# Performance work log

Hardware: AMD Instinct MI355X
Metric: run time of the kernel (lower is better)

The kernel has to match this reference:

```python
import jax, jax.numpy as jnp
import numpy as np

N, E = 50000, 600000
IN_C, HID, OUT_C = 256, 128, 2
R, B, L = 7, 8, 3
ALPHA = 0.1


def _rgcn(x, src, dst, etype, comp, basis, root, bias):
    # comp: [R,B], basis: [B,d,d] -> per-relation weights W: [R,d,d]
    n, d = x.shape
    W = jnp.einsum('rb,bdf->rdf', comp, basis)
    # combined (dst, relation) segment id for per-relation mean aggregation
    seg = dst * R + etype
    msg = x[src]  # [E,d] gather
    s = jax.ops.segment_sum(msg, seg, num_segments=n * R)  # [N*R,d]
    cnt = jax.ops.segment_sum(jnp.ones((E,), x.dtype), seg, num_segments=n * R)
    agg = (s / jnp.maximum(cnt, 1.0)[:, None]).reshape(n, R, d)  # per-relation mean
    return x @ root + bias + jnp.einsum('nrd,rdf->nf', agg, W)


def setup_inputs() -> dict:
    key = jax.random.key(0)
    ks = jax.random.split(key, 10)
    sc = 0.05
    x = jax.random.normal(ks[0], (N, IN_C), dtype=jnp.float32)
    edge_index = jax.random.randint(ks[1], (2, E), 0, N)
    edge_type = jax.random.randint(ks[2], (E,), 0, R)
    # GPR temp init: alpha*(1-alpha)^k, last entry (1-alpha)^K
    temp = jnp.asarray(ALPHA * (1.0 - ALPHA) ** np.arange(L + 1), dtype=jnp.float32)
    temp = temp.at[-1].set((1.0 - ALPHA) ** L)
    lin1_w = jax.random.normal(ks[3], (IN_C, HID), jnp.float32) * sc
    lin1_b = jnp.zeros((HID,), jnp.float32)
    lin2_w = jax.random.normal(ks[4], (HID, OUT_C), jnp.float32) * sc
    lin2_b = jnp.zeros((OUT_C,), jnp.float32)
    comps = jax.random.normal(ks[5], (L, R, B), jnp.float32) * sc
    bases = jax.random.normal(ks[6], (L, B, HID, HID), jnp.float32) * sc
    roots = jax.random.normal(ks[7], (L, HID, HID), jnp.float32) * sc
    conv_biases = jnp.zeros((L, HID), jnp.float32)
    return dict(x=x, edge_index=edge_index, edge_type=edge_type, temp=temp,
                lin1_w=lin1_w, lin1_b=lin1_b, lin2_w=lin2_w, lin2_b=lin2_b,
                comps=comps, bases=bases, roots=roots, conv_biases=conv_biases)


def reference(x, edge_index, edge_type, temp, lin1_w, lin1_b, lin2_w, lin2_b,
              comps, bases, roots, conv_biases):
    src, dst = edge_index[0], edge_index[1]
    h = x @ lin1_w + lin1_b
    hidden = h * temp[0]
    cur = hidden
    for i in range(L):
        cur = _rgcn(cur, src, dst, edge_type, comps[i], bases[i], roots[i], conv_biases[i])
        if i < L - 1:
            cur = jax.nn.relu(cur)  # dropout p=0.4 is identity in eval mode
        hidden = hidden + temp[i + 1] * cur
    return hidden @ lin2_w + lin2_b
```

## Files before the change

### kernel.cpp

```cpp
#include <hip/hip_runtime.h>
#include <cstdint>


constexpr int N_NODES  = 50000;
constexpr int E_EDGES  = 600000;
constexpr int R_REL    = 7;
constexpr int HID      = 128;
constexpr int IN_C     = 256;
constexpr int L_LAYERS = 3;
constexpr int AGG_COLS = 896;
constexpr int K_CAT    = 1024;
constexpr int NR       = N_NODES * R_REL;
constexpr int SCANR_BLOCKS = (NR + 255) / 256;
constexpr int WCAT_ELEMS = L_LAYERS * 128 * K_CAT;

#define DEVI __device__ __forceinline__

using short8  = __attribute__((ext_vector_type(8))) short;
using floatx4 = __attribute__((ext_vector_type(4))) float;

DEVI unsigned short f2bf(float f) {
  unsigned u = __float_as_uint(f);
  unsigned r = (u + 0x7FFFu + ((u >> 16) & 1u)) >> 16;
  return (unsigned short)r;
}
DEVI float bf2f(unsigned short h) { return __uint_as_float(((unsigned)h) << 16); }

__global__ __launch_bounds__(256) void prep_weights(
    const float* __restrict__ w1,
    const float* __restrict__ comps,
    const float* __restrict__ bases,
    const float* __restrict__ roots,
    unsigned short* __restrict__ w1T,
    unsigned short* __restrict__ wcat2T)
{
  int t = blockIdx.x * 256 + threadIdx.x;
  if (t < WCAT_ELEMS) {
    int l   = t >> 17;
    int rem = t & 131071;
    int f   = rem >> 10;
    int k   = rem & 1023;
    float v;
    if (k < 128) {
      v = roots[((size_t)l * 128 + k) * 128 + f];
    } else {
      int r = (k - 128) >> 7, d = (k - 128) & 127;
      const float* cp = comps + ((size_t)l * R_REL + r) * 8;
      const float* bp = bases + (((size_t)l * 8) * 128 + d) * 128 + f;
      float s = 0.f;
#pragma unroll
      for (int b = 0; b < 8; ++b) s += cp[b] * bp[(size_t)b * 128 * 128];
      v = s;
    }
    wcat2T[t] = f2bf(v);
  } else {
    int u = t - WCAT_ELEMS;
    if (u < HID * IN_C) {
      int m = u >> 8, k = u & 255;
      w1T[m * IN_C + k] = f2bf(w1[k * HID + m]);
    }
  }
}

__global__ __launch_bounds__(256) void hist_kernel(
    const int* __restrict__ ei, const int* __restrict__ et,
    int* __restrict__ cntRel, int* __restrict__ erank)
{
  int e = blockIdx.x * 256 + threadIdx.x;
  if (e >= E_EDGES) return;
  int seg = ei[E_EDGES + e] * R_REL + et[e];
  erank[e] = atomicAdd(&cntRel[seg], 1);
}

__global__ __launch_bounds__(256) void scanA_kernel(
    const int* __restrict__ cnt, int* __restrict__ tmpOff,
    int* __restrict__ blockSums)
{
  __shared__ int s[256];
  int i = blockIdx.x * 256 + threadIdx.x;
  int v = (i < NR) ? cnt[i] : 0;
  s[threadIdx.x] = v;
  __syncthreads();
#pragma unroll
  for (int d = 1; d < 256; d <<= 1) {
    int t = (threadIdx.x >= d) ? s[threadIdx.x - d] : 0;
    __syncthreads();
    s[threadIdx.x] += t;
    __syncthreads();
  }
  if (i < NR) tmpOff[i] = s[threadIdx.x] - v;
  if (threadIdx.x == 255) blockSums[blockIdx.x] = s[255];
}

__global__ __launch_bounds__(256) void scanB_kernel(int* __restrict__ bs)
{
  __shared__ int s[256];
  __shared__ int carry;
  if (threadIdx.x == 0) carry = 0;
  __syncthreads();
  for (int base = 0; base < SCANR_BLOCKS; base += 256) {
    int cOld = carry;
    int i = base + threadIdx.x;
    int v = (i < SCANR_BLOCKS) ? bs[i] : 0;
    s[threadIdx.x] = v;
    __syncthreads();
#pragma unroll
    for (int d = 1; d < 256; d <<= 1) {
      int t = (threadIdx.x >= d) ? s[threadIdx.x - d] : 0;
      __syncthreads();
      s[threadIdx.x] += t;
      __syncthreads();
    }
    if (i < SCANR_BLOCKS) bs[i] = s[threadIdx.x] - v + cOld;
    __syncthreads();
    if (threadIdx.x == 0) carry = cOld + s[255];
    __syncthreads();
  }
}

__global__ __launch_bounds__(256) void scanC_kernel(
    const int* __restrict__ tmpOff, const int* __restrict__ blockSums,
    int* __restrict__ drs)
{
  int i = blockIdx.x * 256 + threadIdx.x;
  if (i < NR) drs[i] = tmpOff[i] + blockSums[blockIdx.x];
  if (i == 0) drs[NR] = E_EDGES;
}

__global__ __launch_bounds__(256) void place_kernel(
    const int* __restrict__ ei, const int* __restrict__ et,
    const int* __restrict__ drs, const int* __restrict__ erank,
    unsigned short* __restrict__ esrc)
{
  int e = blockIdx.x * 256 + threadIdx.x;
  if (e >= E_EDGES) return;
  int seg = ei[E_EDGES + e] * R_REL + et[e];
  int pos = drs[seg] + erank[e];
  esrc[pos] = (unsigned short)ei[e];
}

constexpr int AGG_NPF = 16;
__global__ __launch_bounds__(256) void agg_reg_kernel(
    const unsigned short* __restrict__ curA,
    const unsigned short* __restrict__ esrc,
    const int* __restrict__ drs,
    unsigned short* __restrict__ aggB)
{
  const int tid  = threadIdx.x;
  const int lane = tid & 63;
  const int dst  = blockIdx.x * 4 + (tid >> 6);
  if (dst >= N_NODES) return;
  const int segBase = dst * R_REL;

  int bnd = drs[segBase + (lane & 7)];
  const int a0    = __shfl(bnd, 0);
  const int total = __shfl(bnd, 7) - a0;

  int pk = 0;
  if (lane < total) pk = (int)esrc[a0 + lane];

  const unsigned* colp = (const unsigned*)curA + lane;
  unsigned* outp = (unsigned*)(aggB + (size_t)dst * AGG_COLS) + lane;

  int r = 0;
  int segStart = 0;
  int segEnd = __shfl(bnd, 1) - a0;
  float sx = 0.f, sy = 0.f;
  int pos = 0;

#define AGG_FLUSH()                                                        \
  while (r < R_REL && segEnd == pos) {                                     \
    int c = segEnd - segStart;                                             \
    float sc = (c > 0) ? 1.0f / (float)c : 0.f;                            \
    unsigned pck = (unsigned)f2bf(sx * sc) | ((unsigned)f2bf(sy * sc) << 16); \
    outp[r * 64] = pck;                                                    \
    sx = 0.f; sy = 0.f;                                                    \
    segStart = segEnd;                                                     \
    ++r;                                                                   \
    segEnd = (r < R_REL) ? (__shfl(bnd, r + 1) - a0) : 0x7FFFFFFF;         \
  }

  AGG_FLUSH();

  for (int base = 0; base < total; base += AGG_NPF) {
    const int cnt = min(total - base, AGG_NPF);
    unsigned v[AGG_NPF];
#pragma unroll
    for (int e = 0; e < AGG_NPF; ++e) {
      if (e < cnt) {
        int idx = base + e;
        int src = (idx < 64) ? __shfl(pk, idx) : (int)esrc[a0 + idx];
        v[e] = colp[src * 64];
      }
    }
#pragma unroll
    for (int e = 0; e < AGG_NPF; ++e) {
      if (e >= cnt) break;
      unsigned u = v[e];
      sx += __uint_as_float(u << 16);
      sy += __uint_as_float(u & 0xFFFF0000u);
      ++pos;
      AGG_FLUSH();
    }
  }
#undef AGG_FLUSH
}

__global__ __launch_bounds__(256) void gemm_lin1(
    const float* __restrict__ x,
    const unsigned short* __restrict__ BT,
    const float* __restrict__ bias,
    const float* __restrict__ temp,
    unsigned short* __restrict__ b0out)
{
  __shared__ unsigned short Atile[64][136];
  __shared__ unsigned short Btile[128][136];
  const int tid  = threadIdx.x;
  const int row0 = blockIdx.x * 64;
  const int lane = tid & 63;
  const int wid  = tid >> 6;
  const int wrow = (wid & 1) * 32;
  const int wcol = (wid >> 1) * 64;
  const int l15  = lane & 15;
  const int quad = lane >> 4;

  floatx4 acc[2][4] = {};

  for (int k0 = 0; k0 < IN_C; k0 += 128) {
#pragma unroll
    for (int it = 0; it < 4; ++it) {
      int chunk = it * 256 + tid;
      int r = chunk >> 4, cc = (chunk & 15) << 3;
      int grow = row0 + r;
      uint4 va = make_uint4(0u, 0u, 0u, 0u);
      if (grow < N_NODES) {
        const float* xp = x + (size_t)grow * IN_C + k0 + cc;
        float4 f0 = *(const float4*)xp;
        float4 f1 = *(const float4*)(xp + 4);
        va.x = (unsigned)f2bf(f0.x) | ((unsigned)f2bf(f0.y) << 16);
        va.y = (unsigned)f2bf(f0.z) | ((unsigned)f2bf(f0.w) << 16);
        va.z = (unsigned)f2bf(f1.x) | ((unsigned)f2bf(f1.y) << 16);
        va.w = (unsigned)f2bf(f1.z) | ((unsigned)f2bf(f1.w) << 16);
      }
      *(uint4*)(&Atile[r][cc]) = va;
    }
#pragma unroll
    for (int it = 0; it < 8; ++it) {
      int chunk = it * 256 + tid;
      int n = chunk >> 4, cc = (chunk & 15) << 3;
      *(uint4*)(&Btile[n][cc]) =
          *(const uint4*)(BT + (size_t)n * IN_C + k0 + cc);
    }
    __syncthreads();
#pragma unroll
    for (int ks = 0; ks < 4; ++ks) {
      int kc = ks * 32 + quad * 8;
      short8 af[2], bfr[4];
#pragma unroll
      for (int i = 0; i < 2; ++i)
        af[i] = *(const short8*)(&Atile[wrow + i * 16 + l15][kc]);
#pragma unroll
      for (int j = 0; j < 4; ++j)
        bfr[j] = *(const short8*)(&Btile[wcol + j * 16 + l15][kc]);
#pragma unroll
      for (int i = 0; i < 2; ++i)
#pragma unroll
        for (int j = 0; j < 4; ++j)
          acc[i][j] = __builtin_amdgcn_mfma_f32_16x16x32_bf16(
              af[i], bfr[j], acc[i][j], 0, 0, 0);
    }
    __syncthreads();
  }

  float t0 = temp[0];
#pragma unroll
  for (int i = 0; i < 2; ++i) {
    int lrow0 = wrow + i * 16 + quad * 4;
#pragma unroll
    for (int j = 0; j < 4; ++j) {
      int gcol = wcol + j * 16 + l15;
      float bb = bias[gcol];
#pragma unroll
      for (int r = 0; r < 4; ++r)
        Atile[lrow0 + r][gcol] = f2bf(t0 * (acc[i][j][r] + bb));
    }
  }
  __syncthreads();
#pragma unroll
  for (int it = 0; it < 4; ++it) {
    int chunk = it * 256 + tid;
    int r = chunk >> 4, cc = (chunk & 15) << 3;
    int grow = row0 + r;
    if (grow < N_NODES)
      *(uint4*)(b0out + (size_t)grow * HID + cc) = *(const uint4*)(&Atile[r][cc]);
  }
}

__global__ __launch_bounds__(256) void gemm_layer(
    const unsigned short* __restrict__ curA,
    const unsigned short* __restrict__ aggB,
    const unsigned short* __restrict__ BT,
    const float* __restrict__ bias,
    unsigned short* __restrict__ bout,
    int layer)
{
  __shared__ unsigned short Btile[128][136];
  const int tid  = threadIdx.x;
  const int row0 = blockIdx.x * 128;
  const int lane = tid & 63;
  const int wid  = tid >> 6;
  const int wrow = (wid & 1) * 64;
  const int wcol = (wid >> 1) * 64;
  const int l15  = lane & 15;
  const int quad = lane >> 4;

  floatx4 acc[4][4] = {};

  for (int p = 0; p < 8; ++p) {
#pragma unroll
    for (int it = 0; it < 8; ++it) {
      int chunk = it * 256 + tid;
      int n = chunk >> 4, cc = (chunk & 15) << 3;
      *(uint4*)(&Btile[n][cc]) =
          *(const uint4*)(BT + (size_t)n * K_CAT + p * 128 + cc);
    }
    __syncthreads();
#pragma unroll
    for (int ks = 0; ks < 4; ++ks) {
      int kc = ks * 32 + quad * 8;
      short8 af[4], bfr[4];
#pragma unroll
      for (int i = 0; i < 4; ++i) {
        int grow = row0 + wrow + i * 16 + l15;
        short8 v = {};
        if (grow < N_NODES) {
          const unsigned short* ap = (p == 0)
              ? curA + (size_t)grow * HID + kc
              : aggB + (size_t)grow * AGG_COLS + (p - 1) * 128 + kc;
          v = *(const short8*)ap;
        }
        af[i] = v;
      }
#pragma unroll
      for (int j = 0; j < 4; ++j)
        bfr[j] = *(const short8*)(&Btile[wcol + j * 16 + l15][kc]);
#pragma unroll
      for (int i = 0; i < 4; ++i)
#pragma unroll
        for (int j = 0; j < 4; ++j)
          acc[i][j] = __builtin_amdgcn_mfma_f32_16x16x32_bf16(
              af[i], bfr[j], acc[i][j], 0, 0, 0);
    }
    __syncthreads();
  }

  const bool isLast = (layer == L_LAYERS - 1);
#pragma unroll
  for (int i = 0; i < 4; ++i) {
    int lrow0 = wrow + i * 16 + quad * 4;
#pragma unroll
    for (int j = 0; j < 4; ++j) {
      int gcol = wcol + j * 16 + l15;
      float bb = bias[gcol];
#pragma unroll
      for (int r = 0; r < 4; ++r) {
        float c = acc[i][j][r] + bb;
        if (!isLast) c = fmaxf(c, 0.f);
        Btile[lrow0 + r][gcol] = f2bf(c);
      }
    }
  }
  __syncthreads();
#pragma unroll
  for (int it = 0; it < 8; ++it) {
    int chunk = it * 256 + tid;
    int r = chunk >> 4, cc = (chunk & 15) << 3;
    int grow = row0 + r;
    if (grow < N_NODES)
      *(uint4*)(bout + (size_t)grow * HID + cc) = *(const uint4*)(&Btile[r][cc]);
  }
}

__global__ __launch_bounds__(256) void final_kernel(
    const unsigned short* __restrict__ b0, const unsigned short* __restrict__ b1,
    const unsigned short* __restrict__ b2v, const unsigned short* __restrict__ b3,
    const float* __restrict__ temp,
    const float* __restrict__ w2, const float* __restrict__ b2bias,
    float* __restrict__ out)
{
  int node = blockIdx.x * 4 + (threadIdx.x >> 6);
  int lane = threadIdx.x & 63;
  if (node >= N_NODES) return;
  float t1 = temp[1], t2 = temp[2], t3 = temp[3];
  size_t base = (size_t)node * 64 + lane;
  unsigned u0 = ((const unsigned*)b0)[base];
  unsigned u1 = ((const unsigned*)b1)[base];
  unsigned u2 = ((const unsigned*)b2v)[base];
  unsigned u3 = ((const unsigned*)b3)[base];
  float hx = bf2f((unsigned short)(u0 & 0xFFFF)) +
             t1 * bf2f((unsigned short)(u1 & 0xFFFF)) +
             t2 * bf2f((unsigned short)(u2 & 0xFFFF)) +
             t3 * bf2f((unsigned short)(u3 & 0xFFFF));
  float hy = bf2f((unsigned short)(u0 >> 16)) +
             t1 * bf2f((unsigned short)(u1 >> 16)) +
             t2 * bf2f((unsigned short)(u2 >> 16)) +
             t3 * bf2f((unsigned short)(u3 >> 16));
  int d0 = lane * 2, d1 = lane * 2 + 1;
  float a0 = hx * w2[d0 * 2 + 0] + hy * w2[d1 * 2 + 0];
  float a1 = hx * w2[d0 * 2 + 1] + hy * w2[d1 * 2 + 1];
#pragma unroll
  for (int off = 32; off > 0; off >>= 1) {
    a0 += __shfl_down(a0, off);
    a1 += __shfl_down(a1, off);
  }
  if (lane == 0) {
    out[node * 2 + 0] = a0 + b2bias[0];
    out[node * 2 + 1] = a1 + b2bias[1];
  }
}

extern "C" void kernel_launch(void* const* d_in, const int* in_sizes, int n_in,
                              void* d_out, int out_size, void* d_ws, size_t ws_size,
                              hipStream_t stream) {
  const float* x     = (const float*)d_in[0];
  const int*   ei    = (const int*)d_in[1];
  const int*   et    = (const int*)d_in[2];
  const float* temp  = (const float*)d_in[3];
  const float* w1    = (const float*)d_in[4];
  const float* b1    = (const float*)d_in[5];
  const float* w2    = (const float*)d_in[6];
  const float* b2    = (const float*)d_in[7];
  const float* comps = (const float*)d_in[8];
  const float* bases = (const float*)d_in[9];
  const float* roots = (const float*)d_in[10];
  const float* cbias = (const float*)d_in[11];

  char* ws = (char*)d_ws;
  size_t off = 0;
  auto take = [&](size_t bytes) {
    char* p = ws + off;
    off = (off + bytes + 255) & ~(size_t)255;
    return p;
  };
  unsigned short* wcat2T = (unsigned short*)take((size_t)WCAT_ELEMS * 2);
  unsigned short* w1T    = (unsigned short*)take((size_t)HID * IN_C * 2);
  int*   cntRel  = (int*)take((size_t)NR * 4);
  int*   tmpOffR = (int*)take((size_t)NR * 4);
  int*   blockSumsR = (int*)take((size_t)SCANR_BLOCKS * 4);
  int*   drs     = (int*)take((size_t)(NR + 1) * 4);
  int*   erank   = (int*)take((size_t)E_EDGES * 4);
  unsigned short* esrc = (unsigned short*)take((size_t)E_EDGES * 2);
  unsigned short* bl[L_LAYERS + 1];
  for (int i = 0; i <= L_LAYERS; ++i)
    bl[i] = (unsigned short*)take((size_t)N_NODES * HID * 2);
  unsigned short* aggB = (unsigned short*)take((size_t)N_NODES * AGG_COLS * 2);

  hipMemsetAsync(cntRel, 0, (size_t)NR * 4, stream);

  hipLaunchKernelGGL(prep_weights,
                     dim3((WCAT_ELEMS + HID * IN_C + 255) / 256), dim3(256),
                     0, stream, w1, comps, bases, roots, w1T, wcat2T);
  hipLaunchKernelGGL(hist_kernel, dim3((E_EDGES + 255) / 256), dim3(256), 0,
                     stream, ei, et, cntRel, erank);
  hipLaunchKernelGGL(scanA_kernel, dim3(SCANR_BLOCKS), dim3(256), 0, stream,
                     cntRel, tmpOffR, blockSumsR);
  hipLaunchKernelGGL(scanB_kernel, dim3(1), dim3(256), 0, stream, blockSumsR);
  hipLaunchKernelGGL(scanC_kernel, dim3(SCANR_BLOCKS), dim3(256), 0, stream,
                     tmpOffR, blockSumsR, drs);
  hipLaunchKernelGGL(place_kernel, dim3((E_EDGES + 255) / 256), dim3(256), 0,
                     stream, ei, et, drs, erank, esrc);

  const int rowBlocks64  = (N_NODES + 63) / 64;
  const int rowBlocks128 = (N_NODES + 127) / 128;
  hipLaunchKernelGGL(gemm_lin1, dim3(rowBlocks64), dim3(256), 0, stream,
                     x, w1T, b1, temp, bl[0]);

  for (int l = 0; l < L_LAYERS; ++l) {
    hipLaunchKernelGGL(agg_reg_kernel, dim3((N_NODES + 3) / 4), dim3(256),
                       0, stream, bl[l], esrc, drs, aggB);
    hipLaunchKernelGGL(gemm_layer, dim3(rowBlocks128), dim3(256), 0, stream,
                       bl[l], aggB, wcat2T + (size_t)l * 128 * K_CAT,
                       cbias + (size_t)l * HID, bl[l + 1], l);
  }

  hipLaunchKernelGGL(final_kernel, dim3((N_NODES + 3) / 4), dim3(256), 0, stream,
                     bl[0], bl[1], bl[2], bl[3], temp, w2, b2, (float*)d_out);
}
```

Before: 478.6 us.

## Transform-then-gather: apply relation weights before aggregating edge messages

Swaps the order of the RGCN layer. Instead of aggregating per-relation means into an N x 896 buffer and running a K=1024 GEMM, each layer first computes the root and seven per-relation transforms (eight N x 128 outputs), then gathers with precomputed per-edge offset and 1/count weight. The root term and bias are added during the gather, which also drops the 896-wide aggregate write and reread. The cost is writing and reading an 8 x N x 128 intermediate and 8-byte edge records instead of 2-byte source ids.

```diff
diff --git a/kernel.cpp b/kernel.cpp
--- a/kernel.cpp
+++ b/kernel.cpp
@@ -8,11 +8,9 @@
 constexpr int HID      = 128;
 constexpr int IN_C     = 256;
 constexpr int L_LAYERS = 3;
-constexpr int AGG_COLS = 896;
-constexpr int K_CAT    = 1024;
 constexpr int NR       = N_NODES * R_REL;
 constexpr int SCANR_BLOCKS = (NR + 255) / 256;
-constexpr int WCAT_ELEMS = L_LAYERS * 128 * K_CAT;
+constexpr int WSLAB_ELEMS = L_LAYERS * 8 * 128 * 128;
 
 #define DEVI __device__ __forceinline__
 
@@ -32,29 +30,31 @@
     const float* __restrict__ bases,
     const float* __restrict__ roots,
     unsigned short* __restrict__ w1T,
-    unsigned short* __restrict__ wcat2T)
+    unsigned short* __restrict__ wslabT)
 {
   int t = blockIdx.x * 256 + threadIdx.x;
-  if (t < WCAT_ELEMS) {
-    int l   = t >> 17;
-    int rem = t & 131071;
-    int f   = rem >> 10;
-    int k   = rem & 1023;
+  if (t < WSLAB_ELEMS) {
+    int l    = t >> 17;
+    int rem  = t & 131071;
+    int s    = rem >> 14;
+    int rem2 = rem & 16383;
+    int f    = rem2 >> 7;
+    int k    = rem2 & 127;
     float v;
-    if (k < 128) {
+    if (s == 0) {
       v = roots[((size_t)l * 128 + k) * 128 + f];
     } else {
-      int r = (k - 128) >> 7, d = (k - 128) & 127;
+      int r = s - 1;
       const float* cp = comps + ((size_t)l * R_REL + r) * 8;
-      const float* bp = bases + (((size_t)l * 8) * 128 + d) * 128 + f;
-      float s = 0.f;
-#pragma unroll
-      for (int b = 0; b < 8; ++b) s += cp[b] * bp[(size_t)b * 128 * 128];
-      v = s;
-    }
-    wcat2T[t] = f2bf(v);
+      const float* bp = bases + (((size_t)l * 8) * 128 + k) * 128 + f;
+      float sacc = 0.f;
+#pragma unroll
+      for (int b = 0; b < 8; ++b) sacc += cp[b] * bp[(size_t)b * 128 * 128];
+      v = sacc;
+    }
+    wslabT[t] = f2bf(v);
   } else {
-    int u = t - WCAT_ELEMS;
+    int u = t - WSLAB_ELEMS;
     if (u < HID * IN_C) {
       int m = u >> 8, k = u & 255;
       w1T[m * IN_C + k] = f2bf(w1[k * HID + m]);
@@ -130,80 +130,18 @@
 __global__ __launch_bounds__(256) void place_kernel(
     const int* __restrict__ ei, const int* __restrict__ et,
     const int* __restrict__ drs, const int* __restrict__ erank,
-    unsigned short* __restrict__ esrc)
+    const int* __restrict__ cntRel,
+    uint2* __restrict__ eoffw)
 {
   int e = blockIdx.x * 256 + threadIdx.x;
   if (e >= E_EDGES) return;
-  int seg = ei[E_EDGES + e] * R_REL + et[e];
+  int src = ei[e];
+  int rel = et[e];
+  int seg = ei[E_EDGES + e] * R_REL + rel;
   int pos = drs[seg] + erank[e];
-  esrc[pos] = (unsigned short)ei[e];
-}
-
-constexpr int AGG_NPF = 16;
-__global__ __launch_bounds__(256) void agg_reg_kernel(
-    const unsigned short* __restrict__ curA,
-    const unsigned short* __restrict__ esrc,
-    const int* __restrict__ drs,
-    unsigned short* __restrict__ aggB)
-{
-  const int tid  = threadIdx.x;
-  const int lane = tid & 63;
-  const int dst  = blockIdx.x * 4 + (tid >> 6);
-  if (dst >= N_NODES) return;
-  const int segBase = dst * R_REL;
-
-  int bnd = drs[segBase + (lane & 7)];
-  const int a0    = __shfl(bnd, 0);
-  const int total = __shfl(bnd, 7) - a0;
-
-  int pk = 0;
-  if (lane < total) pk = (int)esrc[a0 + lane];
-
-  const unsigned* colp = (const unsigned*)curA + lane;
-  unsigned* outp = (unsigned*)(aggB + (size_t)dst * AGG_COLS) + lane;
-
-  int r = 0;
-  int segStart = 0;
-  int segEnd = __shfl(bnd, 1) - a0;
-  float sx = 0.f, sy = 0.f;
-  int pos = 0;
-
-#define AGG_FLUSH()                                                        \
-  while (r < R_REL && segEnd == pos) {                                     \
-    int c = segEnd - segStart;                                             \
-    float sc = (c > 0) ? 1.0f / (float)c : 0.f;                            \
-    unsigned pck = (unsigned)f2bf(sx * sc) | ((unsigned)f2bf(sy * sc) << 16); \
-    outp[r * 64] = pck;                                                    \
-    sx = 0.f; sy = 0.f;                                                    \
-    segStart = segEnd;                                                     \
-    ++r;                                                                   \
-    segEnd = (r < R_REL) ? (__shfl(bnd, r + 1) - a0) : 0x7FFFFFFF;         \
-  }
-
-  AGG_FLUSH();
-
-  for (int base = 0; base < total; base += AGG_NPF) {
-    const int cnt = min(total - base, AGG_NPF);
-    unsigned v[AGG_NPF];
-#pragma unroll
-    for (int e = 0; e < AGG_NPF; ++e) {
-      if (e < cnt) {
-        int idx = base + e;
-        int src = (idx < 64) ? __shfl(pk, idx) : (int)esrc[a0 + idx];
-        v[e] = colp[src * 64];
-      }
-    }
-#pragma unroll
-    for (int e = 0; e < AGG_NPF; ++e) {
-      if (e >= cnt) break;
-      unsigned u = v[e];
-      sx += __uint_as_float(u << 16);
-      sy += __uint_as_float(u & 0xFFFF0000u);
-      ++pos;
-      AGG_FLUSH();
-    }
-  }
-#undef AGG_FLUSH
+  unsigned off = ((1u + (unsigned)rel) * (unsigned)N_NODES + (unsigned)src) * 64u;
+  float w = 1.0f / (float)cntRel[seg];
+  eoffw[pos] = make_uint2(off, __float_as_uint(w));
 }
 
 __global__ __launch_bounds__(256) void gemm_lin1(
@@ -296,17 +234,15 @@
   }
 }
 
-__global__ __launch_bounds__(256) void gemm_layer(
+__global__ __launch_bounds__(256) void tg_kernel(
     const unsigned short* __restrict__ curA,
-    const unsigned short* __restrict__ aggB,
-    const unsigned short* __restrict__ BT,
-    const float* __restrict__ bias,
-    unsigned short* __restrict__ bout,
-    int layer)
+    const unsigned short* __restrict__ WT,
+    unsigned short* __restrict__ T)
 {
   __shared__ unsigned short Btile[128][136];
   const int tid  = threadIdx.x;
   const int row0 = blockIdx.x * 128;
+  const int s    = blockIdx.y;
   const int lane = tid & 63;
   const int wid  = tid >> 6;
   const int wrow = (wid & 1) * 64;
@@ -314,71 +250,126 @@
   const int l15  = lane & 15;
   const int quad = lane >> 4;
 
+  const unsigned short* Wp = WT + (size_t)s * 128 * 128;
+
+#pragma unroll
+  for (int it = 0; it < 8; ++it) {
+    int chunk = it * 256 + tid;
+    int n = chunk >> 4, cc = (chunk & 15) << 3;
+    *(uint4*)(&Btile[n][cc]) = *(const uint4*)(Wp + (size_t)n * 128 + cc);
+  }
+  __syncthreads();
+
   floatx4 acc[4][4] = {};
-
-  for (int p = 0; p < 8; ++p) {
-#pragma unroll
-    for (int it = 0; it < 8; ++it) {
-      int chunk = it * 256 + tid;
-      int n = chunk >> 4, cc = (chunk & 15) << 3;
-      *(uint4*)(&Btile[n][cc]) =
-          *(const uint4*)(BT + (size_t)n * K_CAT + p * 128 + cc);
-    }
-    __syncthreads();
-#pragma unroll
-    for (int ks = 0; ks < 4; ++ks) {
-      int kc = ks * 32 + quad * 8;
-      short8 af[4], bfr[4];
-#pragma unroll
-      for (int i = 0; i < 4; ++i) {
-        int grow = row0 + wrow + i * 16 + l15;
-        short8 v = {};
-        if (grow < N_NODES) {
-          const unsigned short* ap = (p == 0)
-              ? curA + (size_t)grow * HID + kc
-              : aggB + (size_t)grow * AGG_COLS + (p - 1) * 128 + kc;
-          v = *(const short8*)ap;
-        }
-        af[i] = v;
-      }
+#pragma unroll
+  for (int ks = 0; ks < 4; ++ks) {
+    int kc = ks * 32 + quad * 8;
+    short8 af[4], bfr[4];
+#pragma unroll
+    for (int i = 0; i < 4; ++i) {
+      int grow = row0 + wrow + i * 16 + l15;
+      short8 v = {};
+      if (grow < N_NODES)
+        v = *(const short8*)(curA + (size_t)grow * HID + kc);
+      af[i] = v;
+    }
+#pragma unroll
+    for (int j = 0; j < 4; ++j)
+      bfr[j] = *(const short8*)(&Btile[wcol + j * 16 + l15][kc]);
+#pragma unroll
+    for (int i = 0; i < 4; ++i)
 #pragma unroll
       for (int j = 0; j < 4; ++j)
-        bfr[j] = *(const short8*)(&Btile[wcol + j * 16 + l15][kc]);
-#pragma unroll
-      for (int i = 0; i < 4; ++i)
-#pragma unroll
-        for (int j = 0; j < 4; ++j)
-          acc[i][j] = __builtin_amdgcn_mfma_f32_16x16x32_bf16(
-              af[i], bfr[j], acc[i][j], 0, 0, 0);
-    }
-    __syncthreads();
-  }
-
-  const bool isLast = (layer == L_LAYERS - 1);
+        acc[i][j] = __builtin_amdgcn_mfma_f32_16x16x32_bf16(
+            af[i], bfr[j], acc[i][j], 0, 0, 0);
+  }
+  __syncthreads();
+
 #pragma unroll
   for (int i = 0; i < 4; ++i) {
     int lrow0 = wrow + i * 16 + quad * 4;
 #pragma unroll
     for (int j = 0; j < 4; ++j) {
       int gcol = wcol + j * 16 + l15;
-      float bb = bias[gcol];
-#pragma unroll
-      for (int r = 0; r < 4; ++r) {
-        float c = acc[i][j][r] + bb;
-        if (!isLast) c = fmaxf(c, 0.f);
-        Btile[lrow0 + r][gcol] = f2bf(c);
-      }
-    }
-  }
-  __syncthreads();
+#pragma unroll
+      for (int r = 0; r < 4; ++r)
+        Btile[lrow0 + r][gcol] = f2bf(acc[i][j][r]);
+    }
+  }
+  __syncthreads();
+  unsigned short* Tout = T + (size_t)s * N_NODES * HID;
 #pragma unroll
   for (int it = 0; it < 8; ++it) {
     int chunk = it * 256 + tid;
     int r = chunk >> 4, cc = (chunk & 15) << 3;
     int grow = row0 + r;
     if (grow < N_NODES)
-      *(uint4*)(bout + (size_t)grow * HID + cc) = *(const uint4*)(&Btile[r][cc]);
-  }
+      *(uint4*)(Tout + (size_t)grow * HID + cc) = *(const uint4*)(&Btile[r][cc]);
+  }
+}
+
+__global__ __launch_bounds__(256) void gather_out(
+    const unsigned short* __restrict__ T,
+    const uint2* __restrict__ eoffw,
+    const int* __restrict__ drs,
+    const float* __restrict__ bias,
+    unsigned short* __restrict__ bout,
+    int layer)
+{
+  const int tid  = threadIdx.x;
+  const int lane = tid & 63;
+  const int dst  = blockIdx.x * 4 + (tid >> 6);
+  if (dst >= N_NODES) return;
+
+  int bd = drs[dst * R_REL + ((lane & 1) ? R_REL : 0)];
+  const int a0    = __shfl(bd, 0);
+  const int total = __shfl(bd, 1) - a0;
+
+  unsigned peo = 0u; int pew = 0;
+  if (lane < total) {
+    uint2 pe = eoffw[a0 + lane];
+    peo = pe.x; pew = (int)pe.y;
+  }
+
+  const unsigned* Td = (const unsigned*)T;
+  float sx = 0.f, sy = 0.f;
+
+  for (int base = 0; base < total; base += 16) {
+    const int cnt = min(total - base, 16);
+    unsigned uval[16]; float uw[16];
+#pragma unroll
+    for (int e = 0; e < 16; ++e) {
+      if (e < cnt) {
+        int idx = base + e;
+        unsigned off; float w;
+        if (idx < 64) {
+          off = (unsigned)__shfl((int)peo, idx);
+          w   = __uint_as_float((unsigned)__shfl(pew, idx));
+        } else {
+          uint2 pe = eoffw[a0 + idx];
+          off = pe.x; w = __uint_as_float(pe.y);
+        }
+        uw[e]   = w;
+        uval[e] = Td[(size_t)off + lane];
+      }
+    }
+#pragma unroll
+    for (int e = 0; e < 16; ++e) {
+      if (e >= cnt) break;
+      unsigned u = uval[e];
+      sx += uw[e] * __uint_as_float(u << 16);
+      sy += uw[e] * __uint_as_float(u & 0xFFFF0000u);
+    }
+  }
+
+  unsigned ur = Td[(size_t)dst * 64 + lane];
+  sx += __uint_as_float(ur << 16);
+  sy += __uint_as_float(ur & 0xFFFF0000u);
+  float2 bb = *(const float2*)(bias + lane * 2);
+  float c0 = sx + bb.x, c1 = sy + bb.y;
+  if (layer < L_LAYERS - 1) { c0 = fmaxf(c0, 0.f); c1 = fmaxf(c1, 0.f); }
+  unsigned pck = (unsigned)f2bf(c0) | ((unsigned)f2bf(c1) << 16);
+  ((unsigned*)bout)[(size_t)dst * 64 + lane] = pck;
 }
 
 __global__ __launch_bounds__(256) void final_kernel(
@@ -442,24 +433,24 @@
     off = (off + bytes + 255) & ~(size_t)255;
     return p;
   };
-  unsigned short* wcat2T = (unsigned short*)take((size_t)WCAT_ELEMS * 2);
+  unsigned short* wslabT = (unsigned short*)take((size_t)WSLAB_ELEMS * 2);
   unsigned short* w1T    = (unsigned short*)take((size_t)HID * IN_C * 2);
   int*   cntRel  = (int*)take((size_t)NR * 4);
   int*   tmpOffR = (int*)take((size_t)NR * 4);
   int*   blockSumsR = (int*)take((size_t)SCANR_BLOCKS * 4);
   int*   drs     = (int*)take((size_t)(NR + 1) * 4);
   int*   erank   = (int*)take((size_t)E_EDGES * 4);
-  unsigned short* esrc = (unsigned short*)take((size_t)E_EDGES * 2);
+  uint2* eoffw   = (uint2*)take((size_t)E_EDGES * 8);
   unsigned short* bl[L_LAYERS + 1];
   for (int i = 0; i <= L_LAYERS; ++i)
     bl[i] = (unsigned short*)take((size_t)N_NODES * HID * 2);
-  unsigned short* aggB = (unsigned short*)take((size_t)N_NODES * AGG_COLS * 2);
+  unsigned short* T = (unsigned short*)take((size_t)8 * N_NODES * HID * 2);
 
   hipMemsetAsync(cntRel, 0, (size_t)NR * 4, stream);
 
   hipLaunchKernelGGL(prep_weights,
-                     dim3((WCAT_ELEMS + HID * IN_C + 255) / 256), dim3(256),
-                     0, stream, w1, comps, bases, roots, w1T, wcat2T);
+                     dim3((WSLAB_ELEMS + HID * IN_C + 255) / 256), dim3(256),
+                     0, stream, w1, comps, bases, roots, w1T, wslabT);
   hipLaunchKernelGGL(hist_kernel, dim3((E_EDGES + 255) / 256), dim3(256), 0,
                      stream, ei, et, cntRel, erank);
   hipLaunchKernelGGL(scanA_kernel, dim3(SCANR_BLOCKS), dim3(256), 0, stream,
@@ -468,7 +459,7 @@
   hipLaunchKernelGGL(scanC_kernel, dim3(SCANR_BLOCKS), dim3(256), 0, stream,
                      tmpOffR, blockSumsR, drs);
   hipLaunchKernelGGL(place_kernel, dim3((E_EDGES + 255) / 256), dim3(256), 0,
-                     stream, ei, et, drs, erank, esrc);
+                     stream, ei, et, drs, erank, cntRel, eoffw);
 
   const int rowBlocks64  = (N_NODES + 63) / 64;
   const int rowBlocks128 = (N_NODES + 127) / 128;
@@ -476,11 +467,11 @@
                      x, w1T, b1, temp, bl[0]);
 
   for (int l = 0; l < L_LAYERS; ++l) {
-    hipLaunchKernelGGL(agg_reg_kernel, dim3((N_NODES + 3) / 4), dim3(256),
-                       0, stream, bl[l], esrc, drs, aggB);
-    hipLaunchKernelGGL(gemm_layer, dim3(rowBlocks128), dim3(256), 0, stream,
-                       bl[l], aggB, wcat2T + (size_t)l * 128 * K_CAT,
-                       cbias + (size_t)l * HID, bl[l + 1], l);
+    hipLaunchKernelGGL(tg_kernel, dim3(rowBlocks128, 8), dim3(256), 0, stream,
+                       bl[l], wslabT + (size_t)l * 8 * 128 * 128, T);
+    hipLaunchKernelGGL(gather_out, dim3((N_NODES + 3) / 4), dim3(256), 0,
+                       stream, T, eoffw, drs, cbias + (size_t)l * HID,
+                       bl[l + 1], l);
   }
 
   hipLaunchKernelGGL(final_kernel, dim3((N_NODES + 3) / 4), dim3(256), 0, stream,
```

Result: no change. 481.5 us (+0.6%).

## Fuse final projection into last GEMM layer and drop scan/memset launches

Applied to the files above, without the earlier changes.

The final GPR combination and output projection are folded into the epilogue of the last gemm_layer, so the layer-3 output is consumed from shared memory instead of being written and re-read. The single-block scanB pass is removed; each scanC block instead reduces the preceding block sums itself. The count-buffer memset moves into prep_weights. This saves launches and a full N×128 write/read, at the cost of redundant block-sum reductions in scanC and a less coalesced per-row read pattern in the fused epilogue (each thread walks 32 words of a row).

```diff
diff --git a/kernel.cpp b/kernel.cpp
--- a/kernel.cpp
+++ b/kernel.cpp
@@ -32,9 +32,11 @@
     const float* __restrict__ bases,
     const float* __restrict__ roots,
     unsigned short* __restrict__ w1T,
-    unsigned short* __restrict__ wcat2T)
+    unsigned short* __restrict__ wcat2T,
+    int* __restrict__ cntRel)
 {
   int t = blockIdx.x * 256 + threadIdx.x;
+  if (t < NR) cntRel[t] = 0;
   if (t < WCAT_ELEMS) {
     int l   = t >> 17;
     int rem = t & 131071;
@@ -92,38 +94,24 @@
   if (threadIdx.x == 255) blockSums[blockIdx.x] = s[255];
 }
 
-__global__ __launch_bounds__(256) void scanB_kernel(int* __restrict__ bs)
-{
-  __shared__ int s[256];
-  __shared__ int carry;
-  if (threadIdx.x == 0) carry = 0;
-  __syncthreads();
-  for (int base = 0; base < SCANR_BLOCKS; base += 256) {
-    int cOld = carry;
-    int i = base + threadIdx.x;
-    int v = (i < SCANR_BLOCKS) ? bs[i] : 0;
-    s[threadIdx.x] = v;
-    __syncthreads();
-#pragma unroll
-    for (int d = 1; d < 256; d <<= 1) {
-      int t = (threadIdx.x >= d) ? s[threadIdx.x - d] : 0;
-      __syncthreads();
-      s[threadIdx.x] += t;
-      __syncthreads();
-    }
-    if (i < SCANR_BLOCKS) bs[i] = s[threadIdx.x] - v + cOld;
-    __syncthreads();
-    if (threadIdx.x == 0) carry = cOld + s[255];
-    __syncthreads();
-  }
-}
-
 __global__ __launch_bounds__(256) void scanC_kernel(
     const int* __restrict__ tmpOff, const int* __restrict__ blockSums,
     int* __restrict__ drs)
 {
-  int i = blockIdx.x * 256 + threadIdx.x;
-  if (i < NR) drs[i] = tmpOff[i] + blockSums[blockIdx.x];
+  __shared__ int red[256];
+  const int bid = blockIdx.x;
+  int part = 0;
+  for (int i = threadIdx.x; i < bid; i += 256) part += blockSums[i];
+  red[threadIdx.x] = part;
+  __syncthreads();
+#pragma unroll
+  for (int d = 128; d > 0; d >>= 1) {
+    if (threadIdx.x < d) red[threadIdx.x] += red[threadIdx.x + d];
+    __syncthreads();
+  }
+  const int base = red[0];
+  int i = bid * 256 + threadIdx.x;
+  if (i < NR) drs[i] = tmpOff[i] + base;
   if (i == 0) drs[NR] = E_EDGES;
 }
 
@@ -302,6 +290,12 @@
     const unsigned short* __restrict__ BT,
     const float* __restrict__ bias,
     unsigned short* __restrict__ bout,
+    const unsigned short* __restrict__ b0g,
+    const unsigned short* __restrict__ b1g,
+    const float* __restrict__ temp,
+    const float* __restrict__ w2,
+    const float* __restrict__ b2bias,
+    float* __restrict__ out,
     int layer)
 {
   __shared__ unsigned short Btile[128][136];
@@ -371,51 +365,48 @@
     }
   }
   __syncthreads();
-#pragma unroll
-  for (int it = 0; it < 8; ++it) {
-    int chunk = it * 256 + tid;
-    int r = chunk >> 4, cc = (chunk & 15) << 3;
+
+  if (!isLast) {
+#pragma unroll
+    for (int it = 0; it < 8; ++it) {
+      int chunk = it * 256 + tid;
+      int r = chunk >> 4, cc = (chunk & 15) << 3;
+      int grow = row0 + r;
+      if (grow < N_NODES)
+        *(uint4*)(bout + (size_t)grow * HID + cc) = *(const uint4*)(&Btile[r][cc]);
+    }
+  } else {
+    float t1 = temp[1], t2 = temp[2], t3 = temp[3];
+    int r = tid >> 1, half = tid & 1;
     int grow = row0 + r;
-    if (grow < N_NODES)
-      *(uint4*)(bout + (size_t)grow * HID + cc) = *(const uint4*)(&Btile[r][cc]);
-  }
-}
-
-__global__ __launch_bounds__(256) void final_kernel(
-    const unsigned short* __restrict__ b0, const unsigned short* __restrict__ b1,
-    const unsigned short* __restrict__ b2v, const unsigned short* __restrict__ b3,
-    const float* __restrict__ temp,
-    const float* __restrict__ w2, const float* __restrict__ b2bias,
-    float* __restrict__ out)
-{
-  int node = blockIdx.x * 4 + (threadIdx.x >> 6);
-  int lane = threadIdx.x & 63;
-  if (node >= N_NODES) return;
-  float t1 = temp[1], t2 = temp[2], t3 = temp[3];
-  size_t base = (size_t)node * 64 + lane;
-  unsigned u0 = ((const unsigned*)b0)[base];
-  unsigned u1 = ((const unsigned*)b1)[base];
-  unsigned u2 = ((const unsigned*)b2v)[base];
-  unsigned u3 = ((const unsigned*)b3)[base];
-  float hx = bf2f((unsigned short)(u0 & 0xFFFF)) +
-             t1 * bf2f((unsigned short)(u1 & 0xFFFF)) +
-             t2 * bf2f((unsigned short)(u2 & 0xFFFF)) +
-             t3 * bf2f((unsigned short)(u3 & 0xFFFF));
-  float hy = bf2f((unsigned short)(u0 >> 16)) +
-             t1 * bf2f((unsigned short)(u1 >> 16)) +
-             t2 * bf2f((unsigned short)(u2 >> 16)) +
-             t3 * bf2f((unsigned short)(u3 >> 16));
-  int d0 = lane * 2, d1 = lane * 2 + 1;
-  float a0 = hx * w2[d0 * 2 + 0] + hy * w2[d1 * 2 + 0];
-  float a1 = hx * w2[d0 * 2 + 1] + hy * w2[d1 * 2 + 1];
-#pragma unroll
-  for (int off = 32; off > 0; off >>= 1) {
-    a0 += __shfl_down(a0, off);
-    a1 += __shfl_down(a1, off);
-  }
-  if (lane == 0) {
-    out[node * 2 + 0] = a0 + b2bias[0];
-    out[node * 2 + 1] = a1 + b2bias[1];
+    float s0 = 0.f, s1 = 0.f;
+    if (grow < N_NODES) {
+      const unsigned* p0 = (const unsigned*)(b0g  + (size_t)grow * HID) + half * 32;
+      const unsigned* p1 = (const unsigned*)(b1g  + (size_t)grow * HID) + half * 32;
+      const unsigned* p2 = (const unsigned*)(curA + (size_t)grow * HID) + half * 32;
+#pragma unroll
+      for (int c = 0; c < 32; ++c) {
+        unsigned u0 = p0[c], u1 = p1[c], u2 = p2[c];
+        unsigned uc = *(const unsigned*)(&Btile[r][half * 64 + c * 2]);
+        float hx = bf2f((unsigned short)(u0 & 0xFFFF)) +
+                   t1 * bf2f((unsigned short)(u1 & 0xFFFF)) +
+                   t2 * bf2f((unsigned short)(u2 & 0xFFFF)) +
+                   t3 * bf2f((unsigned short)(uc & 0xFFFF));
+        float hy = bf2f((unsigned short)(u0 >> 16)) +
+                   t1 * bf2f((unsigned short)(u1 >> 16)) +
+                   t2 * bf2f((unsigned short)(u2 >> 16)) +
+                   t3 * bf2f((unsigned short)(uc >> 16));
+        int d = half * 64 + c * 2;
+        s0 += hx * w2[d * 2 + 0] + hy * w2[(d + 1) * 2 + 0];
+        s1 += hx * w2[d * 2 + 1] + hy * w2[(d + 1) * 2 + 1];
+      }
+    }
+    s0 += __shfl_xor(s0, 1);
+    s1 += __shfl_xor(s1, 1);
+    if (half == 0 && grow < N_NODES) {
+      out[grow * 2 + 0] = s0 + b2bias[0];
+      out[grow * 2 + 1] = s1 + b2bias[1];
+    }
   }
 }
 
@@ -455,16 +446,13 @@
     bl[i] = (unsigned short*)take((size_t)N_NODES * HID * 2);
   unsigned short* aggB = (unsigned short*)take((size_t)N_NODES * AGG_COLS * 2);
 
-  hipMemsetAsync(cntRel, 0, (size_t)NR * 4, stream);
-
   hipLaunchKernelGGL(prep_weights,
                      dim3((WCAT_ELEMS + HID * IN_C + 255) / 256), dim3(256),
-                     0, stream, w1, comps, bases, roots, w1T, wcat2T);
+                     0, stream, w1, comps, bases, roots, w1T, wcat2T, cntRel);
   hipLaunchKernelGGL(hist_kernel, dim3((E_EDGES + 255) / 256), dim3(256), 0,
                      stream, ei, et, cntRel, erank);
   hipLaunchKernelGGL(scanA_kernel, dim3(SCANR_BLOCKS), dim3(256), 0, stream,
                      cntRel, tmpOffR, blockSumsR);
-  hipLaunchKernelGGL(scanB_kernel, dim3(1), dim3(256), 0, stream, blockSumsR);
   hipLaunchKernelGGL(scanC_kernel, dim3(SCANR_BLOCKS), dim3(256), 0, stream,
                      tmpOffR, blockSumsR, drs);
   hipLaunchKernelGGL(place_kernel, dim3((E_EDGES + 255) / 256), dim3(256), 0,
@@ -480,9 +468,7 @@
                        0, stream, bl[l], esrc, drs, aggB);
     hipLaunchKernelGGL(gemm_layer, dim3(rowBlocks128), dim3(256), 0, stream,
                        bl[l], aggB, wcat2T + (size_t)l * 128 * K_CAT,
-                       cbias + (size_t)l * HID, bl[l + 1], l);
-  }
-
-  hipLaunchKernelGGL(final_kernel, dim3((N_NODES + 3) / 4), dim3(256), 0, stream,
-                     bl[0], bl[1], bl[2], bl[3], temp, w2, b2, (float*)d_out);
-}
+                       cbias + (size_t)l * HID, bl[l + 1],
+                       bl[0], bl[1], temp, w2, b2, (float*)d_out, l);
+  }
+}
```

New measurement: 527.1 us. 10.1% more time.
